# Kernel optimization log

Hardware: AMD Instinct MI355X
Metric: run time of the kernel (lower is better)

## Reference

```python
import jax, jax.numpy as jnp
import numpy as np

V, S, D, H = 32000, 1024, 768, 3072
EPS = 1e-5


def pos_encoding(seq_len, dim, dtype=jnp.float32):
    # pe[pos, i] = sin(pos/10000^(i/dim)) if i even else cos(pos/10000^(i/dim))
    pos = jnp.arange(seq_len, dtype=dtype)[:, None]
    i = jnp.arange(dim, dtype=dtype)[None, :]
    ang = pos / jnp.power(jnp.asarray(10000.0, dtype), i / dim)
    even = (jnp.arange(dim) % 2 == 0)[None, :]
    return jnp.where(even, jnp.sin(ang), jnp.cos(ang))


def layernorm2d(x, w, b):
    # normalizes over last two dims (token_size, input_dim), affine params [S, D]
    m = jnp.mean(x, axis=(-2, -1), keepdims=True)
    v = jnp.mean((x - m) ** 2, axis=(-2, -1), keepdims=True)
    return (x - m) / jnp.sqrt(v + EPS) * w + b


def setup_inputs() -> dict:
    key = jax.random.key(0)
    ks = jax.random.split(key, 16)
    sc = 0.02
    emb = jax.random.normal(ks[0], (V, D), jnp.float32) * sc
    emb = emb.at[0].set(0.0)  # padding_idx=0
    inp = {
        "x": jax.random.randint(ks[1], (8, S), 0, V),
        "emb": emb,
        "Wq": jax.random.normal(ks[2], (D, H), jnp.float32) * sc,
        "bq": jnp.zeros((H,), jnp.float32),
        "Wk": jax.random.normal(ks[3], (D, H), jnp.float32) * sc,
        "bk": jnp.zeros((H,), jnp.float32),
        "Wv": jax.random.normal(ks[4], (D, H), jnp.float32) * sc,
        "bv": jnp.zeros((H,), jnp.float32),
        "Wo": jax.random.normal(ks[5], (H, D), jnp.float32) * sc,
        "bo": jnp.zeros((D,), jnp.float32),
        "W1": jax.random.normal(ks[6], (D, H), jnp.float32) * sc,
        "b1": jnp.zeros((H,), jnp.float32),
        "W2": jax.random.normal(ks[7], (H, D), jnp.float32) * sc,
        "b2": jnp.zeros((D,), jnp.float32),
        "ln1_w": jnp.ones((S, D), jnp.float32),
        "ln1_b": jnp.zeros((S, D), jnp.float32),
        "ln2_w": jnp.ones((S, D), jnp.float32),
        "ln2_b": jnp.zeros((S, D), jnp.float32),
    }
    return inp


def reference(x, emb, Wq, bq, Wk, bk, Wv, bv, Wo, bo, W1, b1, W2, b2, ln1_w, ln1_b, ln2_w, ln2_b):
    y = emb[x]                                   # [B, S, D]
    y = y + pos_encoding(y.shape[1], y.shape[2], y.dtype)
    # unscaled self-attention (no 1/sqrt(d) factor, faithful to source)
    q = y @ Wq + bq
    k = y @ Wk + bk
    v = y @ Wv + bv
    attn = jax.nn.softmax(jnp.einsum("bsh,bth->bst", q, k), axis=-1)
    a = jnp.einsum("bst,bth->bsh", attn, v) @ Wo + bo
    y = layernorm2d(y + a, ln1_w, ln1_b)
    # FFN: GELU applied AFTER second linear (faithful to source)
    f = jax.nn.gelu((y @ W1 + b1) @ W2 + b2, approximate=False)
    y = layernorm2d(y + f, ln2_w, ln2_b)
    return y
```

## Files before the change

### kernel.cpp

```cpp
#include <hip/hip_runtime.h>
#include <hip/hip_fp16.h>

#define DI __device__ __forceinline__

typedef _Float16 f16x8 __attribute__((ext_vector_type(8)));
typedef float f32x4 __attribute__((ext_vector_type(4)));

struct alignas(8) h4 { __half x, y, z, w; };

DI void async16(const void* g, void* l) {
  __builtin_amdgcn_global_load_lds(
      (__attribute__((address_space(1))) void*)g,
      (__attribute__((address_space(3))) void*)l, 16, 0, 0);
}

DI float waveReduceSum(float v) {
#pragma unroll
  for (int i = 1; i < 64; i <<= 1) v += __shfl_xor(v, i);
  return v;
}
DI float waveReduceMax(float v) {
#pragma unroll
  for (int i = 1; i < 64; i <<= 1) v = fmaxf(v, __shfl_xor(v, i));
  return v;
}

DI float gelu_exact(float x) { return 0.5f * x * (1.f + erff(x * 0.70710678118654752f)); }

template <typename CT, bool BIAS, bool BROW>
__global__ __launch_bounds__(256) void gemm_nt(
    const __half* __restrict__ A, int lda, long long sA,
    const __half* __restrict__ Bt, int ldb, long long sB,
    const float* __restrict__ bias, CT* __restrict__ C, int ldc, long long sC,
    int mT, int nT, int K) {
  __shared__ __align__(16) __half As[128 * 64];
  __shared__ __align__(16) __half Bs[128 * 64];

  const int tid = threadIdx.x;
  const int wave = tid >> 6, lane = tid & 63;

  const int gsz = 8 * nT;
  const int g = blockIdx.x / gsz, r = blockIdx.x % gsz;
  const int m0 = (g * 8 + (r & 7)) * 128;
  const int n0 = (r >> 3) * 128;

  A += (long long)blockIdx.z * sA;
  Bt += (long long)blockIdx.z * sB;
  C += (long long)blockIdx.z * sC;
  const int wm = wave & 1, wn = wave >> 1;

  f32x4 acc[4][4];
#pragma unroll
  for (int i = 0; i < 4; ++i)
#pragma unroll
    for (int j = 0; j < 4; ++j) acc[i][j] = (f32x4){0.f, 0.f, 0.f, 0.f};

  const int srow = tid >> 3;
  const int gc = (tid & 7) ^ (srow & 7);
  const __half* Ag = A + (size_t)(m0 + srow) * lda + gc * 8;
  const __half* Bg = Bt + (size_t)(n0 + srow) * ldb + gc * 8;
  const size_t a32 = (size_t)32 * lda, b32 = (size_t)32 * ldb;
  char* AsW = (char*)As + wave * 1024;
  char* BsW = (char*)Bs + wave * 1024;

  const int ml = lane & 15, q = lane >> 4, lx = lane & 7;

  for (int k0 = 0; k0 < K; k0 += 64) {
#pragma unroll
    for (int i = 0; i < 4; ++i) {
      async16(Ag + i * a32 + k0, AsW + i * 4096);
      async16(Bg + i * b32 + k0, BsW + i * 4096);
    }
    __syncthreads();
#pragma unroll
    for (int j = 0; j < 2; ++j) {
      f16x8 af[4], bf[4];
#pragma unroll
      for (int i = 0; i < 4; ++i) {
        af[i] = *(const f16x8*)(As + ((size_t)(wm * 64 + i * 16 + ml) * 8 + ((q + 4 * j) ^ lx)) * 8);
        bf[i] = *(const f16x8*)(Bs + ((size_t)(wn * 64 + i * 16 + ml) * 8 + ((q + 4 * j) ^ lx)) * 8);
      }
#pragma unroll
      for (int i = 0; i < 4; ++i)
#pragma unroll
        for (int jn = 0; jn < 4; ++jn)
          acc[i][jn] = __builtin_amdgcn_mfma_f32_16x16x32_f16(af[i], bf[jn], acc[i][jn], 0, 0, 0);
    }
    __syncthreads();
  }

#pragma unroll
  for (int j = 0; j < 4; ++j) {
    const int col = n0 + wn * 64 + j * 16 + ml;
    const float bcol = BIAS ? bias[col] : 0.f;
#pragma unroll
    for (int i = 0; i < 4; ++i) {
      const int row = m0 + wm * 64 + i * 16 + q * 4;
#pragma unroll
      for (int rr = 0; rr < 4; ++rr) {
        float v = acc[i][j][rr] + bcol;
        if constexpr (BROW) v += bias[row + rr];
        if constexpr (sizeof(CT) == 4)
          C[(size_t)(row + rr) * ldc + col] = v;
        else
          C[(size_t)(row + rr) * ldc + col] = __float2half(v);
      }
    }
  }
}

__global__ __launch_bounds__(256) void embed_pos_kernel(
    const int* __restrict__ x, const float* __restrict__ emb,
    float* __restrict__ y, __half* __restrict__ yh) {
  const int row = blockIdx.x;
  const int s = row & 1023;
  const int tok = x[row];
  const float* ep = emb + (size_t)tok * 768;
  float* yp = y + (size_t)row * 768;
  __half* hp = yh + (size_t)row * 768;
  const float c = -13.287712379549449f / 768.f;
  for (int d = threadIdx.x; d < 768; d += 256) {
    float ang = (float)s * exp2f((float)d * c);
    float pe = (d & 1) ? cosf(ang) : sinf(ang);
    float v = ep[d] + pe;
    yp[d] = v;
    hp[d] = __float2half(v);
  }
}

__global__ __launch_bounds__(256) void transpose_f32_to_f16(
    const float* __restrict__ in, __half* __restrict__ out, int R, int C) {
  __shared__ float t[32][33];
  const int tx = threadIdx.x & 31, ty = threadIdx.x >> 5;
  const int c = blockIdx.x * 32 + tx;
  const int r0 = blockIdx.y * 32;
#pragma unroll
  for (int i = 0; i < 32; i += 8) t[ty + i][tx] = in[(size_t)(r0 + ty + i) * C + c];
  __syncthreads();
  const int oc = r0 + tx;
  const int o0 = blockIdx.x * 32;
#pragma unroll
  for (int i = 0; i < 32; i += 8)
    out[(size_t)(o0 + ty + i) * R + oc] = __float2half(t[tx][ty + i]);
}

__global__ __launch_bounds__(256) void softmax_rows(
    const float* __restrict__ L, __half* __restrict__ P) {
  const size_t row = blockIdx.x;
  const float4 x = ((const float4*)(L + row * 1024))[threadIdx.x];
  const int wave = threadIdx.x >> 6, lane = threadIdx.x & 63;
  float m = fmaxf(fmaxf(x.x, x.y), fmaxf(x.z, x.w));
  m = waveReduceMax(m);
  __shared__ float sm[4];
  __shared__ float ssum[4];
  if (lane == 0) sm[wave] = m;
  __syncthreads();
  m = fmaxf(fmaxf(sm[0], sm[1]), fmaxf(sm[2], sm[3]));
  float e0 = expf(x.x - m), e1 = expf(x.y - m), e2 = expf(x.z - m), e3 = expf(x.w - m);
  float s = e0 + e1 + e2 + e3;
  s = waveReduceSum(s);
  if (lane == 0) ssum[wave] = s;
  __syncthreads();
  s = ssum[0] + ssum[1] + ssum[2] + ssum[3];
  const float inv = 1.f / s;
  h4 o{__float2half(e0 * inv), __float2half(e1 * inv), __float2half(e2 * inv),
       __float2half(e3 * inv)};
  ((h4*)(P + row * 1024))[threadIdx.x] = o;
}

template <bool GELU>
__global__ __launch_bounds__(256) void residual_stats(
    float* __restrict__ y, const float* __restrict__ a, float2* __restrict__ partials) {
  const int b = blockIdx.y, chunk = blockIdx.x;
  const size_t base = (size_t)b * 786432 + (size_t)chunk * 8192;
  float4* yp = (float4*)(y + base);
  const float4* ap = (const float4*)(a + base);
  float s = 0.f, ss = 0.f;
#pragma unroll
  for (int it = 0; it < 8; ++it) {
    const int idx = it * 256 + threadIdx.x;
    float4 yv = yp[idx];
    float4 av = ap[idx];
    if constexpr (GELU) {
      av.x = gelu_exact(av.x); av.y = gelu_exact(av.y);
      av.z = gelu_exact(av.z); av.w = gelu_exact(av.w);
    }
    float4 r{yv.x + av.x, yv.y + av.y, yv.z + av.z, yv.w + av.w};
    yp[idx] = r;
    s += r.x + r.y + r.z + r.w;
    ss += r.x * r.x + r.y * r.y + r.z * r.z + r.w * r.w;
  }
  s = waveReduceSum(s);
  ss = waveReduceSum(ss);
  __shared__ float2 wr[4];
  const int wave = threadIdx.x >> 6, lane = threadIdx.x & 63;
  if (lane == 0) wr[wave] = make_float2(s, ss);
  __syncthreads();
  if (threadIdx.x == 0) {
    float S = wr[0].x + wr[1].x + wr[2].x + wr[3].x;
    float SS = wr[0].y + wr[1].y + wr[2].y + wr[3].y;
    partials[b * 96 + chunk] = make_float2(S, SS);
  }
}

__global__ __launch_bounds__(64) void ln_finalize(
    const float2* __restrict__ partials, float2* __restrict__ mv) {
  const int b = blockIdx.x;
  const int t = threadIdx.x;
  float2 p = partials[b * 96 + t];
  float s = p.x, ss = p.y;
  if (t + 64 < 96) {
    float2 qq = partials[b * 96 + t + 64];
    s += qq.x;
    ss += qq.y;
  }
  s = waveReduceSum(s);
  ss = waveReduceSum(ss);
  if (t == 0) {
    const float inv = 1.f / 786432.f;
    float mean = s * inv;
    float var = ss * inv - mean * mean;
    mv[b] = make_float2(mean, rsqrtf(var + 1e-5f));
  }
}

template <bool WB>
__global__ __launch_bounds__(256) void ln_apply(
    float* __restrict__ y, __half* __restrict__ yh, const float* __restrict__ w,
    const float* __restrict__ bb, const float2* __restrict__ mv) {
  const unsigned i4 = blockIdx.x * 256 + threadIdx.x;
  const unsigned i = i4 * 4;
  const unsigned b = i / 786432u;
  const unsigned e4 = (i - b * 786432u) >> 2;
  const float2 m = mv[b];
  float4 yv = ((const float4*)y)[i4];
  const float4 wv = ((const float4*)w)[e4];
  const float4 bv = ((const float4*)bb)[e4];
  float4 r;
  r.x = (yv.x - m.x) * m.y * wv.x + bv.x;
  r.y = (yv.y - m.x) * m.y * wv.y + bv.y;
  r.z = (yv.z - m.x) * m.y * wv.z + bv.z;
  r.w = (yv.w - m.x) * m.y * wv.w + bv.w;
  ((float4*)y)[i4] = r;
  if constexpr (WB) {
    h4 o{__float2half(r.x), __float2half(r.y), __float2half(r.z), __float2half(r.w)};
    ((h4*)yh)[i4] = o;
  }
}

extern "C" void kernel_launch(void* const* d_in, const int* in_sizes, int n_in,
                              void* d_out, int out_size, void* d_ws, size_t ws_size,
                              hipStream_t stream) {
  const int* x = (const int*)d_in[0];
  const float* emb = (const float*)d_in[1];
  const float* Wq = (const float*)d_in[2];
  const float* bq = (const float*)d_in[3];
  const float* Wk = (const float*)d_in[4];
  const float* bk = (const float*)d_in[5];
  const float* Wv = (const float*)d_in[6];
  const float* bv = (const float*)d_in[7];
  const float* Wo = (const float*)d_in[8];
  const float* bo = (const float*)d_in[9];
  const float* W1 = (const float*)d_in[10];
  const float* b1 = (const float*)d_in[11];
  const float* W2 = (const float*)d_in[12];
  const float* b2 = (const float*)d_in[13];
  const float* ln1w = (const float*)d_in[14];
  const float* ln1b = (const float*)d_in[15];
  const float* ln2w = (const float*)d_in[16];
  const float* ln2b = (const float*)d_in[17];

  float* y = (float*)d_out;

  char* ws = (char*)d_ws;
  __half* yh = (__half*)(ws + 0);
  __half* qk = (__half*)(ws + 12582912);
  __half* av = qk;
  __half* vT = (__half*)(ws + 113246208);
  float* abuf = (float*)vT;
  float* Lg = (float*)(ws + 163577856);
  __half* Ph = (__half*)(ws + 197132288);
  __half* f1 = (__half*)Lg;
  __half* wslot = (__half*)(ws + 213909504);
  float* bqk = (float*)(ws + 223346688);
  float2* part = (float2*)(ws + 223371264);
  float2* mv = (float2*)(ws + 223377408);
  const size_t WS_NEEDED = 223377472;
  if (ws_size < WS_NEEDED) return;

  const dim3 blk(256);
  const long long SH = 1024LL * 3072, SS = 1024LL * 1024, SY = 1024LL * 768;
  const long long SQK = 1024LL * 6144;

  embed_pos_kernel<<<dim3(8192), blk, 0, stream>>>(x, emb, y, yh);

  transpose_f32_to_f16<<<dim3(96, 24), blk, 0, stream>>>(Wq, wslot, 768, 3072);
  transpose_f32_to_f16<<<dim3(96, 24), blk, 0, stream>>>(Wk, wslot + 3072 * 768, 768, 3072);
  hipMemcpyAsync(bqk, bq, 3072 * 4, hipMemcpyDeviceToDevice, stream);
  hipMemcpyAsync(bqk + 3072, bk, 3072 * 4, hipMemcpyDeviceToDevice, stream);

  gemm_nt<__half, true, false><<<dim3(64 * 48, 1, 1), blk, 0, stream>>>(
      yh, 768, 0, wslot, 768, 0, bqk, qk, 6144, 0, 64, 48, 768);

  transpose_f32_to_f16<<<dim3(96, 24), blk, 0, stream>>>(Wv, wslot, 768, 3072);
  gemm_nt<__half, false, true><<<dim3(24 * 8, 1, 8), blk, 0, stream>>>(
      wslot, 768, 0, yh, 768, SY, bv, vT, 1024, SH, 24, 8, 768);

  gemm_nt<float, false, false><<<dim3(8 * 8, 1, 8), blk, 0, stream>>>(
      qk, 6144, SQK, qk + 3072, 6144, SQK, nullptr, Lg, 1024, SS, 8, 8, 3072);

  softmax_rows<<<dim3(8192), blk, 0, stream>>>(Lg, Ph);

  gemm_nt<__half, false, false><<<dim3(8 * 24, 1, 8), blk, 0, stream>>>(
      Ph, 1024, SS, vT, 1024, SH, nullptr, av, 3072, SH, 8, 24, 1024);

  transpose_f32_to_f16<<<dim3(24, 96), blk, 0, stream>>>(Wo, wslot, 3072, 768);
  gemm_nt<float, true, false><<<dim3(64 * 6, 1, 1), blk, 0, stream>>>(
      av, 3072, 0, wslot, 3072, 0, bo, abuf, 768, 0, 64, 6, 3072);

  residual_stats<false><<<dim3(96, 8), blk, 0, stream>>>(y, abuf, part);
  ln_finalize<<<dim3(8), dim3(64), 0, stream>>>(part, mv);
  ln_apply<true><<<dim3(6144), blk, 0, stream>>>(y, yh, ln1w, ln1b, mv);

  transpose_f32_to_f16<<<dim3(96, 24), blk, 0, stream>>>(W1, wslot, 768, 3072);
  gemm_nt<__half, true, false><<<dim3(64 * 24, 1, 1), blk, 0, stream>>>(
      yh, 768, 0, wslot, 768, 0, b1, f1, 3072, 0, 64, 24, 768);
  transpose_f32_to_f16<<<dim3(24, 96), blk, 0, stream>>>(W2, wslot, 3072, 768);
  gemm_nt<float, true, false><<<dim3(64 * 6, 1, 1), blk, 0, stream>>>(
      f1, 3072, 0, wslot, 3072, 0, b2, abuf, 768, 0, 64, 6, 3072);

  residual_stats<true><<<dim3(96, 8), blk, 0, stream>>>(y, abuf, part);
  ln_finalize<<<dim3(8), dim3(64), 0, stream>>>(part, mv);
  ln_apply<false><<<dim3(6144), blk, 0, stream>>>(y, nullptr, ln2w, ln2b, mv);
}
```

Baseline: 786.3 us.

## Add XCD-aware tile mapping, split-K output GEMMs, merged weight prep, fused LN finalize

Replaces the GEMM block-to-tile mapping with an XCD-aware banded scheme, so blocks landing on the same XCD share operand tiles in its L2. The two K=3072 output projections become 2-way split-K GEMMs over z, and the residual kernel sums the two partial buffers and adds the bias. All weight transposes and bias copies are merged into two prep launches, and ln_finalize is folded into ln_apply, which re-reduces the partials in every block. Q and K are written to separate buffers and the workspace is reorganised, trading extra partial-sum traffic and redundant per-block reductions for fewer launches and more parallelism.

Result: faster. 749.4 us (-4.7%).

```diff
diff --git a/kernel.cpp b/kernel.cpp
--- a/kernel.cpp
+++ b/kernel.cpp
@@ -31,29 +31,35 @@
 __global__ __launch_bounds__(256) void gemm_nt(
     const __half* __restrict__ A, int lda, long long sA,
     const __half* __restrict__ Bt, int ldb, long long sB,
-    const float* __restrict__ bias, CT* __restrict__ C, int ldc, long long sC,
-    int mT, int nT, int K) {
+    const float* __restrict__ bias, long long sBias,
+    CT* __restrict__ C, int ldc, long long sC,
+    int bandN, int nb, int gm, int K) {
   __shared__ __align__(16) __half As[128 * 64];
   __shared__ __align__(16) __half Bs[128 * 64];
 
   const int tid = threadIdx.x;
   const int wave = tid >> 6, lane = tid & 63;
 
-  const int gsz = 8 * nT;
-  const int g = blockIdx.x / gsz, r = blockIdx.x % gsz;
-  const int m0 = (g * 8 + (r & 7)) * 128;
-  const int n0 = (r >> 3) * 128;
+  const int xcd = blockIdx.x & 7;
+  const int j = blockIdx.x >> 3;
+  const int per = nb * gm;
+  const int grp = j / per, rem = j - grp * per;
+  int m, n;
+  if (bandN) { m = grp * gm + rem % gm; n = xcd * nb + rem / gm; }
+  else       { n = grp * gm + rem % gm; m = xcd * nb + rem / gm; }
+  const int m0 = m * 128, n0 = n * 128;
 
   A += (long long)blockIdx.z * sA;
   Bt += (long long)blockIdx.z * sB;
   C += (long long)blockIdx.z * sC;
+  if constexpr (BIAS || BROW) bias += (long long)blockIdx.z * sBias;
   const int wm = wave & 1, wn = wave >> 1;
 
   f32x4 acc[4][4];
 #pragma unroll
   for (int i = 0; i < 4; ++i)
 #pragma unroll
-    for (int j = 0; j < 4; ++j) acc[i][j] = (f32x4){0.f, 0.f, 0.f, 0.f};
+    for (int jj = 0; jj < 4; ++jj) acc[i][jj] = (f32x4){0.f, 0.f, 0.f, 0.f};
 
   const int srow = tid >> 3;
   const int gc = (tid & 7) ^ (srow & 7);
@@ -73,12 +79,12 @@
     }
     __syncthreads();
 #pragma unroll
-    for (int j = 0; j < 2; ++j) {
+    for (int jj = 0; jj < 2; ++jj) {
       f16x8 af[4], bf[4];
 #pragma unroll
       for (int i = 0; i < 4; ++i) {
-        af[i] = *(const f16x8*)(As + ((size_t)(wm * 64 + i * 16 + ml) * 8 + ((q + 4 * j) ^ lx)) * 8);
-        bf[i] = *(const f16x8*)(Bs + ((size_t)(wn * 64 + i * 16 + ml) * 8 + ((q + 4 * j) ^ lx)) * 8);
+        af[i] = *(const f16x8*)(As + ((size_t)(wm * 64 + i * 16 + ml) * 8 + ((q + 4 * jj) ^ lx)) * 8);
+        bf[i] = *(const f16x8*)(Bs + ((size_t)(wn * 64 + i * 16 + ml) * 8 + ((q + 4 * jj) ^ lx)) * 8);
       }
 #pragma unroll
       for (int i = 0; i < 4; ++i)
@@ -90,15 +96,15 @@
   }
 
 #pragma unroll
-  for (int j = 0; j < 4; ++j) {
-    const int col = n0 + wn * 64 + j * 16 + ml;
+  for (int jj = 0; jj < 4; ++jj) {
+    const int col = n0 + wn * 64 + jj * 16 + ml;
     const float bcol = BIAS ? bias[col] : 0.f;
 #pragma unroll
     for (int i = 0; i < 4; ++i) {
       const int row = m0 + wm * 64 + i * 16 + q * 4;
 #pragma unroll
       for (int rr = 0; rr < 4; ++rr) {
-        float v = acc[i][j][rr] + bcol;
+        float v = acc[i][jj][rr] + bcol;
         if constexpr (BROW) v += bias[row + rr];
         if constexpr (sizeof(CT) == 4)
           C[(size_t)(row + rr) * ldc + col] = v;
@@ -107,6 +113,58 @@
       }
     }
   }
+}
+
+__global__ __launch_bounds__(256) void prep1(
+    const float* __restrict__ Wq, const float* __restrict__ Wk,
+    const float* __restrict__ Wv, const float* __restrict__ W1,
+    const float* __restrict__ bq, const float* __restrict__ bk,
+    __half* __restrict__ wA, __half* __restrict__ wB, __half* __restrict__ wC,
+    float* __restrict__ bqk) {
+  if (blockIdx.x == 2304) {
+    if (blockIdx.y == 0)
+      for (int i = threadIdx.x; i < 3072; i += 256) {
+        bqk[i] = bq[i];
+        bqk[3072 + i] = bk[i];
+      }
+    return;
+  }
+  const float* in;
+  __half* out;
+  switch (blockIdx.y) {
+    case 0: in = Wq; out = wA; break;
+    case 1: in = Wk; out = wA + 3072 * 768; break;
+    case 2: in = Wv; out = wB; break;
+    default: in = W1; out = wC; break;
+  }
+  __shared__ float t[32][33];
+  const int tx = threadIdx.x & 31, ty = threadIdx.x >> 5;
+  const int cb = blockIdx.x % 96, rb = blockIdx.x / 96;
+  const int c = cb * 32 + tx, r0 = rb * 32;
+#pragma unroll
+  for (int i = 0; i < 32; i += 8) t[ty + i][tx] = in[(size_t)(r0 + ty + i) * 3072 + c];
+  __syncthreads();
+  const int oc = r0 + tx, o0 = cb * 32;
+#pragma unroll
+  for (int i = 0; i < 32; i += 8)
+    out[(size_t)(o0 + ty + i) * 768 + oc] = __float2half(t[tx][ty + i]);
+}
+
+__global__ __launch_bounds__(256) void prep2(
+    const float* __restrict__ Wo, const float* __restrict__ W2, __half* __restrict__ wA) {
+  const float* in = blockIdx.y ? W2 : Wo;
+  __half* out = wA + (blockIdx.y ? 3072 * 768 : 0);
+  __shared__ float t[32][33];
+  const int tx = threadIdx.x & 31, ty = threadIdx.x >> 5;
+  const int cb = blockIdx.x % 24, rb = blockIdx.x / 24;
+  const int c = cb * 32 + tx, r0 = rb * 32;
+#pragma unroll
+  for (int i = 0; i < 32; i += 8) t[ty + i][tx] = in[(size_t)(r0 + ty + i) * 768 + c];
+  __syncthreads();
+  const int oc = r0 + tx, o0 = cb * 32;
+#pragma unroll
+  for (int i = 0; i < 32; i += 8)
+    out[(size_t)(o0 + ty + i) * 3072 + oc] = __float2half(t[tx][ty + i]);
 }
 
 __global__ __launch_bounds__(256) void embed_pos_kernel(
@@ -128,22 +186,6 @@
   }
 }
 
-__global__ __launch_bounds__(256) void transpose_f32_to_f16(
-    const float* __restrict__ in, __half* __restrict__ out, int R, int C) {
-  __shared__ float t[32][33];
-  const int tx = threadIdx.x & 31, ty = threadIdx.x >> 5;
-  const int c = blockIdx.x * 32 + tx;
-  const int r0 = blockIdx.y * 32;
-#pragma unroll
-  for (int i = 0; i < 32; i += 8) t[ty + i][tx] = in[(size_t)(r0 + ty + i) * C + c];
-  __syncthreads();
-  const int oc = r0 + tx;
-  const int o0 = blockIdx.x * 32;
-#pragma unroll
-  for (int i = 0; i < 32; i += 8)
-    out[(size_t)(o0 + ty + i) * R + oc] = __float2half(t[tx][ty + i]);
-}
-
 __global__ __launch_bounds__(256) void softmax_rows(
     const float* __restrict__ L, __half* __restrict__ P) {
   const size_t row = blockIdx.x;
@@ -170,22 +212,29 @@
 
 template <bool GELU>
 __global__ __launch_bounds__(256) void residual_stats(
-    float* __restrict__ y, const float* __restrict__ a, float2* __restrict__ partials) {
+    float* __restrict__ y, const float* __restrict__ p0, const float* __restrict__ p1,
+    const float* __restrict__ bias, float2* __restrict__ partials) {
   const int b = blockIdx.y, chunk = blockIdx.x;
   const size_t base = (size_t)b * 786432 + (size_t)chunk * 8192;
   float4* yp = (float4*)(y + base);
-  const float4* ap = (const float4*)(a + base);
+  const float4* a0 = (const float4*)(p0 + base);
+  const float4* a1 = (const float4*)(p1 + base);
   float s = 0.f, ss = 0.f;
 #pragma unroll
   for (int it = 0; it < 8; ++it) {
     const int idx = it * 256 + threadIdx.x;
+    const int d = (chunk * 8192 + it * 1024 + threadIdx.x * 4) % 768;
     float4 yv = yp[idx];
-    float4 av = ap[idx];
+    float4 v0 = a0[idx];
+    float4 v1 = a1[idx];
+    const float4 bv = *(const float4*)(bias + d);
+    float ax = v0.x + v1.x + bv.x, ay = v0.y + v1.y + bv.y;
+    float az = v0.z + v1.z + bv.z, aw = v0.w + v1.w + bv.w;
     if constexpr (GELU) {
-      av.x = gelu_exact(av.x); av.y = gelu_exact(av.y);
-      av.z = gelu_exact(av.z); av.w = gelu_exact(av.w);
+      ax = gelu_exact(ax); ay = gelu_exact(ay);
+      az = gelu_exact(az); aw = gelu_exact(aw);
     }
-    float4 r{yv.x + av.x, yv.y + av.y, yv.z + av.z, yv.w + av.w};
+    float4 r{yv.x + ax, yv.y + ay, yv.z + az, yv.w + aw};
     yp[idx] = r;
     s += r.x + r.y + r.z + r.w;
     ss += r.x * r.x + r.y * r.y + r.z * r.z + r.w * r.w;
@@ -203,44 +252,40 @@
   }
 }
 
-__global__ __launch_bounds__(64) void ln_finalize(
-    const float2* __restrict__ partials, float2* __restrict__ mv) {
-  const int b = blockIdx.x;
-  const int t = threadIdx.x;
-  float2 p = partials[b * 96 + t];
-  float s = p.x, ss = p.y;
-  if (t + 64 < 96) {
-    float2 qq = partials[b * 96 + t + 64];
-    s += qq.x;
-    ss += qq.y;
-  }
-  s = waveReduceSum(s);
-  ss = waveReduceSum(ss);
-  if (t == 0) {
-    const float inv = 1.f / 786432.f;
-    float mean = s * inv;
-    float var = ss * inv - mean * mean;
-    mv[b] = make_float2(mean, rsqrtf(var + 1e-5f));
-  }
-}
-
 template <bool WB>
 __global__ __launch_bounds__(256) void ln_apply(
     float* __restrict__ y, __half* __restrict__ yh, const float* __restrict__ w,
-    const float* __restrict__ bb, const float2* __restrict__ mv) {
+    const float* __restrict__ bb, const float2* __restrict__ partials) {
   const unsigned i4 = blockIdx.x * 256 + threadIdx.x;
   const unsigned i = i4 * 4;
   const unsigned b = i / 786432u;
+  const int tid = threadIdx.x;
+  float s = 0.f, ss = 0.f;
+  if (tid < 96) {
+    float2 p = partials[b * 96 + tid];
+    s = p.x;
+    ss = p.y;
+  }
+  s = waveReduceSum(s);
+  ss = waveReduceSum(ss);
+  __shared__ float2 wsum[4];
+  if ((tid & 63) == 0) wsum[tid >> 6] = make_float2(s, ss);
+  __syncthreads();
+  const float S = wsum[0].x + wsum[1].x + wsum[2].x + wsum[3].x;
+  const float SS = wsum[0].y + wsum[1].y + wsum[2].y + wsum[3].y;
+  const float inv = 1.f / 786432.f;
+  const float mean = S * inv;
+  const float rstd = rsqrtf(SS * inv - mean * mean + 1e-5f);
+
   const unsigned e4 = (i - b * 786432u) >> 2;
-  const float2 m = mv[b];
   float4 yv = ((const float4*)y)[i4];
   const float4 wv = ((const float4*)w)[e4];
   const float4 bv = ((const float4*)bb)[e4];
   float4 r;
-  r.x = (yv.x - m.x) * m.y * wv.x + bv.x;
-  r.y = (yv.y - m.x) * m.y * wv.y + bv.y;
-  r.z = (yv.z - m.x) * m.y * wv.z + bv.z;
-  r.w = (yv.w - m.x) * m.y * wv.w + bv.w;
+  r.x = (yv.x - mean) * rstd * wv.x + bv.x;
+  r.y = (yv.y - mean) * rstd * wv.y + bv.y;
+  r.z = (yv.z - mean) * rstd * wv.z + bv.z;
+  r.w = (yv.w - mean) * rstd * wv.w + bv.w;
   ((float4*)y)[i4] = r;
   if constexpr (WB) {
     h4 o{__float2half(r.x), __float2half(r.y), __float2half(r.z), __float2half(r.w)};
@@ -274,62 +319,54 @@
 
   char* ws = (char*)d_ws;
   __half* yh = (__half*)(ws + 0);
-  __half* qk = (__half*)(ws + 12582912);
-  __half* av = qk;
+  __half* qb = (__half*)(ws + 12582912);
+  __half* kb = (__half*)(ws + 62914560);
+  __half* Ph = kb;
   __half* vT = (__half*)(ws + 113246208);
   float* abuf = (float*)vT;
   float* Lg = (float*)(ws + 163577856);
-  __half* Ph = (__half*)(ws + 197132288);
-  __half* f1 = (__half*)Lg;
-  __half* wslot = (__half*)(ws + 213909504);
-  float* bqk = (float*)(ws + 223346688);
-  float2* part = (float2*)(ws + 223371264);
-  float2* mv = (float2*)(ws + 223377408);
-  const size_t WS_NEEDED = 223377472;
+  __half* wA = (__half*)(ws + 197132288);
+  __half* wB = (__half*)(ws + 206569472);
+  __half* wC = (__half*)(ws + 211288064);
+  float* bqk = (float*)(ws + 216006656);
+  float2* part = (float2*)(ws + 216031232);
+  const size_t WS_NEEDED = 216037440;
   if (ws_size < WS_NEEDED) return;
 
   const dim3 blk(256);
-  const long long SH = 1024LL * 3072, SS = 1024LL * 1024, SY = 1024LL * 768;
-  const long long SQK = 1024LL * 6144;
-
+  const long long SH = 1024LL * 3072, SS = 1024LL * 1024;
+  const long long HALF = 25165824;
+  float* p1 = abuf + 6291456;
+
+  prep1<<<dim3(2305, 4), blk, 0, stream>>>(Wq, Wk, Wv, W1, bq, bk, wA, wB, wC, bqk);
   embed_pos_kernel<<<dim3(8192), blk, 0, stream>>>(x, emb, y, yh);
 
-  transpose_f32_to_f16<<<dim3(96, 24), blk, 0, stream>>>(Wq, wslot, 768, 3072);
-  transpose_f32_to_f16<<<dim3(96, 24), blk, 0, stream>>>(Wk, wslot + 3072 * 768, 768, 3072);
-  hipMemcpyAsync(bqk, bq, 3072 * 4, hipMemcpyDeviceToDevice, stream);
-  hipMemcpyAsync(bqk + 3072, bk, 3072 * 4, hipMemcpyDeviceToDevice, stream);
-
-  gemm_nt<__half, true, false><<<dim3(64 * 48, 1, 1), blk, 0, stream>>>(
-      yh, 768, 0, wslot, 768, 0, bqk, qk, 6144, 0, 64, 48, 768);
-
-  transpose_f32_to_f16<<<dim3(96, 24), blk, 0, stream>>>(Wv, wslot, 768, 3072);
-  gemm_nt<__half, false, true><<<dim3(24 * 8, 1, 8), blk, 0, stream>>>(
-      wslot, 768, 0, yh, 768, SY, bv, vT, 1024, SH, 24, 8, 768);
-
-  gemm_nt<float, false, false><<<dim3(8 * 8, 1, 8), blk, 0, stream>>>(
-      qk, 6144, SQK, qk + 3072, 6144, SQK, nullptr, Lg, 1024, SS, 8, 8, 3072);
+  gemm_nt<__half, true, false><<<dim3(1536, 1, 2), blk, 0, stream>>>(
+      yh, 768, 0, wA, 768, 3072LL * 768, bqk, 3072, qb, 3072, HALF, 1, 3, 8, 768);
+  prep2<<<dim3(2304, 2), blk, 0, stream>>>(Wo, W2, wA);
+
+  gemm_nt<__half, false, true><<<dim3(192, 1, 8), blk, 0, stream>>>(
+      wB, 768, 0, yh, 768, 1024LL * 768, bv, 0, vT, 1024, SH, 0, 3, 8, 768);
+
+  gemm_nt<float, false, false><<<dim3(64, 1, 8), blk, 0, stream>>>(
+      qb, 3072, SH, kb, 3072, SH, nullptr, 0, Lg, 1024, SS, 1, 1, 8, 3072);
 
   softmax_rows<<<dim3(8192), blk, 0, stream>>>(Lg, Ph);
 
-  gemm_nt<__half, false, false><<<dim3(8 * 24, 1, 8), blk, 0, stream>>>(
-      Ph, 1024, SS, vT, 1024, SH, nullptr, av, 3072, SH, 8, 24, 1024);
-
-  transpose_f32_to_f16<<<dim3(24, 96), blk, 0, stream>>>(Wo, wslot, 3072, 768);
-  gemm_nt<float, true, false><<<dim3(64 * 6, 1, 1), blk, 0, stream>>>(
-      av, 3072, 0, wslot, 3072, 0, bo, abuf, 768, 0, 64, 6, 3072);
-
-  residual_stats<false><<<dim3(96, 8), blk, 0, stream>>>(y, abuf, part);
-  ln_finalize<<<dim3(8), dim3(64), 0, stream>>>(part, mv);
-  ln_apply<true><<<dim3(6144), blk, 0, stream>>>(y, yh, ln1w, ln1b, mv);
-
-  transpose_f32_to_f16<<<dim3(96, 24), blk, 0, stream>>>(W1, wslot, 768, 3072);
-  gemm_nt<__half, true, false><<<dim3(64 * 24, 1, 1), blk, 0, stream>>>(
-      yh, 768, 0, wslot, 768, 0, b1, f1, 3072, 0, 64, 24, 768);
-  transpose_f32_to_f16<<<dim3(24, 96), blk, 0, stream>>>(W2, wslot, 3072, 768);
-  gemm_nt<float, true, false><<<dim3(64 * 6, 1, 1), blk, 0, stream>>>(
-      f1, 3072, 0, wslot, 3072, 0, b2, abuf, 768, 0, 64, 6, 3072);
-
-  residual_stats<true><<<dim3(96, 8), blk, 0, stream>>>(y, abuf, part);
-  ln_finalize<<<dim3(8), dim3(64), 0, stream>>>(part, mv);
-  ln_apply<false><<<dim3(6144), blk, 0, stream>>>(y, nullptr, ln2w, ln2b, mv);
-}
+  gemm_nt<__half, false, false><<<dim3(192, 1, 8), blk, 0, stream>>>(
+      Ph, 1024, SS, vT, 1024, SH, nullptr, 0, (__half*)qb, 3072, SH, 1, 3, 8, 1024);
+
+  gemm_nt<float, false, false><<<dim3(384, 1, 2), blk, 0, stream>>>(
+      (__half*)qb, 3072, 1536, wA, 3072, 1536, nullptr, 0, abuf, 768, 6291456, 0, 8, 6, 1536);
+
+  residual_stats<false><<<dim3(96, 8), blk, 0, stream>>>(y, abuf, p1, bo, part);
+  ln_apply<true><<<dim3(6144), blk, 0, stream>>>(y, yh, ln1w, ln1b, part);
+
+  gemm_nt<__half, true, false><<<dim3(1536, 1, 1), blk, 0, stream>>>(
+      yh, 768, 0, wC, 768, 0, b1, 0, (__half*)qb, 3072, 0, 1, 3, 8, 768);
+  gemm_nt<float, false, false><<<dim3(384, 1, 2), blk, 0, stream>>>(
+      (__half*)qb, 3072, 1536, wA + 3072 * 768, 3072, 1536, nullptr, 0, abuf, 768, 6291456, 0, 8, 6, 1536);
+
+  residual_stats<true><<<dim3(96, 8), blk, 0, stream>>>(y, abuf, p1, b2, part);
+  ln_apply<false><<<dim3(6144), blk, 0, stream>>>(y, nullptr, ln2w, ln2b, part);
+}
```
